# Kernel tuning notes

Measured on AMD Instinct MI355X. Metric: run time of the kernel, lower is better.

Reference implementation:

```python
import jax, jax.numpy as jnp
import numpy as np

N_NODES = 100000
N_EDGES = 1600000
IN = 128
HID = 128
OUT_CLS = 40
EPS = 1e-12


def setup_inputs() -> dict:
    key = jax.random.key(0)
    ks = jax.random.split(key, 12)
    feat = jax.random.normal(ks[0], (N_NODES, IN), dtype=jnp.float32)
    edge_index = jax.random.randint(ks[1], (2, N_EDGES), 0, N_NODES, dtype=jnp.int64)

    def xavier(k, shape):
        fan_out, fan_in = shape
        lim = float(np.sqrt(6.0 / (fan_in + fan_out)))
        return jax.random.uniform(k, shape, jnp.float32, -lim, lim)

    return {
        "feat": feat,
        "edge_index": edge_index,
        "Wl1": xavier(ks[2], (HID, IN)),  "bl1": jnp.zeros((HID,), jnp.float32), "Wr1": xavier(ks[3], (HID, IN)),
        "Wl2": xavier(ks[4], (HID, HID)), "bl2": jnp.zeros((HID,), jnp.float32), "Wr2": xavier(ks[5], (HID, HID)),
        "Wl3": xavier(ks[6], (HID, HID)), "bl3": jnp.zeros((HID,), jnp.float32), "Wr3": xavier(ks[7], (HID, HID)),
        "Wfc": xavier(ks[8], (OUT_CLS, HID)), "bfc": jnp.zeros((OUT_CLS,), jnp.float32),
    }


def sage_conv(x, src, dst, Wl, bl, Wr):
    # mean-aggregate neighbor messages x[src] into dst nodes (PyG aggr='mean')
    agg = jax.ops.segment_sum(x[src], dst, num_segments=N_NODES)        # [N, d]
    cnt = jax.ops.segment_sum(jnp.ones((src.shape[0],), x.dtype), dst,
                              num_segments=N_NODES)                      # [N]
    agg = agg / jnp.maximum(cnt, 1.0)[:, None]
    out = agg @ Wl.T + bl + x @ Wr.T                                     # lin_l(agg) + lin_r(x)
    # F.normalize(p=2, dim=-1, eps=1e-12)
    norm = jnp.linalg.norm(out, axis=-1, keepdims=True)
    return out / jnp.maximum(norm, EPS)


def reference(feat, edge_index, Wl1, bl1, Wr1, Wl2, bl2, Wr2, Wl3, bl3, Wr3, Wfc, bfc):
    src, dst = edge_index[0], edge_index[1]
    h = jax.nn.relu(sage_conv(feat, src, dst, Wl1, bl1, Wr1))
    h = jax.nn.relu(sage_conv(h, src, dst, Wl2, bl2, Wr2))
    h = sage_conv(h, src, dst, Wl3, bl3, Wr3)
    logits = h @ Wfc.T + bfc
    return jax.nn.softmax(logits, axis=-1)
```

## Files before the change

kernel.cpp:

```cpp
#include <hip/hip_runtime.h>
#include <cstdint>

#define N_NODES 100000
#define N_EDGES 1600000
#define F 128
#define OUT_CLS 40
#define LW 13
#define LBM (LW * 32)
#define BSHIFT 10
#define NBUCK 98
#define TILE 2048

using f32x16 = __attribute__((ext_vector_type(16))) float;
using bf16x8 = __attribute__((ext_vector_type(8))) short;
using f16x2 = __attribute__((ext_vector_type(2))) _Float16;

__device__ __forceinline__ int edge_val(const int* eb, int is64, long idx) {
  return is64 ? eb[2 * idx] : eb[idx];
}

__global__ void k_detect(const unsigned int* eb, int* flag) {
  if (threadIdx.x == 0 && blockIdx.x == 0) {
    int is64 = 1;
#pragma unroll
    for (int i = 1; i < 16; i += 2) is64 &= (eb[i] == 0u);
    flag[0] = is64;
  }
}

#define CH_E 16
__global__ __launch_bounds__(256) void k_chist(const int* __restrict__ eb, const int* __restrict__ flag,
                                               int* __restrict__ bhist) {
  __shared__ int lh[NBUCK];
  int t = threadIdx.x;
  if (t < NBUCK) lh[t] = 0;
  __syncthreads();
  int is64 = flag[0];
  long base = (long)blockIdx.x * (256 * CH_E);
#pragma unroll
  for (int i = 0; i < CH_E; ++i) {
    long e = base + (long)i * 256 + t;
    if (e < N_EDGES) {
      int d = edge_val(eb, is64, (long)N_EDGES + e);
      atomicAdd(&lh[d >> BSHIFT], 1);
    }
  }
  __syncthreads();
  if (t < NBUCK && lh[t]) atomicAdd(&bhist[t], lh[t]);
}

__global__ __launch_bounds__(128) void k_bscan(const int* __restrict__ bhist, int* __restrict__ boff,
                                               int* __restrict__ bkt_cursor, int* __restrict__ off) {
  __shared__ int sh[128];
  int t = threadIdx.x;
  int v = (t < NBUCK) ? bhist[t] : 0;
  sh[t] = v;
  __syncthreads();
  for (int d = 1; d < 128; d <<= 1) {
    int u = (t >= d) ? sh[t - d] : 0;
    __syncthreads();
    sh[t] += u;
    __syncthreads();
  }
  int incl = sh[t];
  if (t < NBUCK) {
    boff[t] = incl - v;
    bkt_cursor[t] = incl - v;
  }
  if (t == NBUCK - 1) boff[NBUCK] = incl;
  if (t == 0) off[N_NODES] = N_EDGES;
}

__global__ __launch_bounds__(256) void k_bscatter(const int* __restrict__ eb, const int* __restrict__ flag,
                                                  int* __restrict__ bkt_cursor, unsigned* __restrict__ ebuf) {
  __shared__ int lhist[128];
  __shared__ int lbase[128];
  __shared__ int gbase[NBUCK];
  __shared__ int lcnt[NBUCK];
  __shared__ unsigned buf[TILE];
  __shared__ int slotpos[TILE];
  int t = threadIdx.x;
  long e0 = (long)blockIdx.x * TILE;
  int is64 = flag[0];
  if (t < 128) lhist[t] = 0;
  __syncthreads();
#pragma unroll
  for (int i = 0; i < TILE / 256; ++i) {
    long e = e0 + t + i * 256;
    if (e < N_EDGES) {
      int d = edge_val(eb, is64, (long)N_EDGES + e);
      atomicAdd(&lhist[d >> BSHIFT], 1);
    }
  }
  __syncthreads();
  if (t < 128) lbase[t] = lhist[t];
  __syncthreads();
  for (int d = 1; d < 128; d <<= 1) {
    int v = (t >= d && t < 128) ? lbase[t - d] : 0;
    __syncthreads();
    if (t < 128) lbase[t] += v;
    __syncthreads();
  }
  if (t < NBUCK) {
    gbase[t] = atomicAdd(&bkt_cursor[t], lhist[t]);
    lcnt[t] = 0;
  }
  __syncthreads();
#pragma unroll
  for (int i = 0; i < TILE / 256; ++i) {
    long e = e0 + t + i * 256;
    if (e < N_EDGES) {
      int d = edge_val(eb, is64, (long)N_EDGES + e);
      int s = edge_val(eb, is64, e);
      int b = d >> BSHIFT;
      int n = atomicAdd(&lcnt[b], 1);
      int slot = lbase[b] - lhist[b] + n;
      buf[slot] = (unsigned)s | ((unsigned)(d & 1023) << 17);
      slotpos[slot] = gbase[b] + n;
    }
  }
  __syncthreads();
  int tile_n = (int)min((long)TILE, (long)N_EDGES - e0);
  for (int i = t; i < tile_n; i += 256) {
    ebuf[slotpos[i]] = buf[i];
  }
}

__global__ __launch_bounds__(1024) void k_fsort(const unsigned* __restrict__ ebuf, const int* __restrict__ boff,
                                                int* __restrict__ off, int* __restrict__ srcs) {
  __shared__ int hist[1024];
  __shared__ int cur[1024];
  __shared__ int wsum[16];
  int b = blockIdx.x;
  int t = threadIdx.x;
  int p0 = boff[b], p1 = boff[b + 1];
  hist[t] = 0;
  __syncthreads();
  for (int p = p0 + t; p < p1; p += 1024) {
    int d = (int)(ebuf[p] >> 17);
    atomicAdd(&hist[d], 1);
  }
  __syncthreads();
  int h = hist[t];
  int v = h;
#pragma unroll
  for (int o = 1; o < 64; o <<= 1) {
    int u = __shfl_up(v, o);
    if ((t & 63) >= o) v += u;
  }
  if ((t & 63) == 63) wsum[t >> 6] = v;
  __syncthreads();
  if (t < 64) {
    int w = (t < 16) ? wsum[t] : 0;
#pragma unroll
    for (int o = 1; o < 16; o <<= 1) {
      int u = __shfl_up(w, o);
      if (t >= o) w += u;
    }
    if (t < 16) wsum[t] = w;
  }
  __syncthreads();
  int base = (t >> 6) ? wsum[(t >> 6) - 1] : 0;
  int gpos = p0 + base + v - h;
  int node = (b << BSHIFT) + t;
  if (node < N_NODES) off[node] = gpos;
  cur[t] = gpos;
  __syncthreads();
  for (int p = p0 + t; p < p1; p += 1024) {
    unsigned e = ebuf[p];
    int pos = atomicAdd(&cur[(int)(e >> 17)], 1);
    srcs[pos] = (int)(e & 0x1FFFFu);
  }
}

__global__ __launch_bounds__(256) void k_tohalf(const float* __restrict__ in, _Float16* __restrict__ o) {
  int i = blockIdx.x * 256 + threadIdx.x;
  if (i >= N_NODES * F / 8) return;
  float4 a = reinterpret_cast<const float4*>(in)[2 * i];
  float4 b = reinterpret_cast<const float4*>(in)[2 * i + 1];
  union {
    _Float16 h[8];
    uint4 u;
  } r;
  r.h[0] = (_Float16)a.x; r.h[1] = (_Float16)a.y; r.h[2] = (_Float16)a.z; r.h[3] = (_Float16)a.w;
  r.h[4] = (_Float16)b.x; r.h[5] = (_Float16)b.y; r.h[6] = (_Float16)b.z; r.h[7] = (_Float16)b.w;
  reinterpret_cast<uint4*>(o)[i] = r.u;
}

__global__ __launch_bounds__(256) void k_aggregate(const _Float16* __restrict__ x, const int* __restrict__ off,
                                                   const int* __restrict__ srcs, float* __restrict__ agg) {
  int n = blockIdx.x * 4 + (threadIdx.x >> 6);
  if (n >= N_NODES) return;
  int l = threadIdx.x & 63;
  int p0 = off[n], p1 = off[n + 1];
  int deg = p1 - p0;
  float sx = 0.f, sy = 0.f;

  for (int base = 0; base < deg; base += 64) {
    int rem = deg - base;
    int cnt = (rem < 64) ? rem : 64;
    int my = (l < cnt) ? srcs[p0 + base + l] : 0;
    int j = 0;
    for (; j + 7 < cnt; j += 8) {
      int s[8];
#pragma unroll
      for (int k = 0; k < 8; ++k) s[k] = __builtin_amdgcn_readlane(my, j + k);
      f16x2 v[8];
#pragma unroll
      for (int k = 0; k < 8; ++k)
        v[k] = *reinterpret_cast<const f16x2*>(x + (size_t)(unsigned)s[k] * F + 2 * l);
#pragma unroll
      for (int k = 0; k < 8; ++k) {
        sx += (float)v[k][0];
        sy += (float)v[k][1];
      }
    }
    for (; j + 3 < cnt; j += 4) {
      int s[4];
#pragma unroll
      for (int k = 0; k < 4; ++k) s[k] = __builtin_amdgcn_readlane(my, j + k);
      f16x2 v[4];
#pragma unroll
      for (int k = 0; k < 4; ++k)
        v[k] = *reinterpret_cast<const f16x2*>(x + (size_t)(unsigned)s[k] * F + 2 * l);
#pragma unroll
      for (int k = 0; k < 4; ++k) {
        sx += (float)v[k][0];
        sy += (float)v[k][1];
      }
    }
    for (; j < cnt; ++j) {
      int s = __builtin_amdgcn_readlane(my, j);
      f16x2 v = *reinterpret_cast<const f16x2*>(x + (size_t)(unsigned)s * F + 2 * l);
      sx += (float)v[0];
      sy += (float)v[1];
    }
  }

  float inv = 1.0f / (float)max(deg, 1);
  float2 r;
  r.x = sx * inv;
  r.y = sy * inv;
  *reinterpret_cast<float2*>(agg + (size_t)n * F + 2 * l) = r;
}

__device__ __forceinline__ void split_pack(const float4& a, const float4& b, bf16x8& hi, bf16x8& lo) {
  float f[8] = {a.x, a.y, a.z, a.w, b.x, b.y, b.z, b.w};
#pragma unroll
  for (int i = 0; i < 8; ++i) {
    union { float f; unsigned u; } u0;
    u0.f = f[i];
    hi[i] = (short)(u0.u >> 16);
    union { unsigned u; float f; } uh;
    uh.u = u0.u & 0xFFFF0000u;
    union { float f; unsigned u; } ur;
    ur.f = f[i] - uh.f;
    lo[i] = (short)(ur.u >> 16);
  }
}

__global__ __launch_bounds__(256) void k_wsplit(const float* __restrict__ Wl1, const float* __restrict__ Wr1,
                                                const float* __restrict__ Wl2, const float* __restrict__ Wr2,
                                                const float* __restrict__ Wl3, const float* __restrict__ Wr3,
                                                unsigned short* __restrict__ wsp) {
  int e = blockIdx.x * 256 + threadIdx.x;
  if (e >= 3 * 16384) return;
  int L = e >> 14, off = e & 16383;
  const float* wl = (L == 0) ? Wl1 : (L == 1) ? Wl2 : Wl3;
  const float* wr = (L == 0) ? Wr1 : (L == 1) ? Wr2 : Wr3;
  unsigned short* base = wsp + (size_t)L * 4 * 16384;
  {
    union { float f; unsigned u; } u0;
    u0.f = wl[off];
    union { unsigned u; float f; } uh;
    uh.u = u0.u & 0xFFFF0000u;
    union { float f; unsigned u; } ur;
    ur.f = u0.f - uh.f;
    base[off] = (unsigned short)(u0.u >> 16);
    base[16384 + off] = (unsigned short)(ur.u >> 16);
  }
  {
    union { float f; unsigned u; } u0;
    u0.f = wr[off];
    union { unsigned u; float f; } uh;
    uh.u = u0.u & 0xFFFF0000u;
    union { float f; unsigned u; } ur;
    ur.f = u0.f - uh.f;
    base[2 * 16384 + off] = (unsigned short)(u0.u >> 16);
    base[3 * 16384 + off] = (unsigned short)(ur.u >> 16);
  }
}

__global__ __launch_bounds__(832, 1) void k_linear(const float* __restrict__ agg, const float* __restrict__ x,
                                                   const unsigned short* __restrict__ wsp,
                                                   const float* __restrict__ bl, float* out,
                                                   _Float16* __restrict__ out16, int relu) {
  __shared__ unsigned short wlds[4][128][136];
  int tid = threadIdx.x;

  for (int c = tid; c < 4 * 2048; c += 832) {
    int m = c >> 11, rem = c & 2047;
    int j = rem >> 4, kc = (rem & 15) * 8;
    uint4 v = *reinterpret_cast<const uint4*>(wsp + (size_t)m * 16384 + j * 128 + kc);
    *reinterpret_cast<uint4*>(&wlds[m][j][kc]) = v;
  }
  __syncthreads();

  int wid = tid >> 6, lane = tid & 63;
  int l31 = lane & 31, lhi = lane >> 5;
  long rb = (long)blockIdx.x * LBM + (long)wid * 32;
  if (rb >= N_NODES) return;

  int r0 = (int)min(rb + l31, (long)N_NODES - 1);
  const float* a0p = agg + (size_t)r0 * F + lhi * 8;
  const float* x0p = x + (size_t)r0 * F + lhi * 8;

  f32x16 acc[4];
#pragma unroll
  for (int ct = 0; ct < 4; ++ct) acc[ct] = (f32x16)0.f;

  float4 ap = *reinterpret_cast<const float4*>(a0p);
  float4 aq = *reinterpret_cast<const float4*>(a0p + 4);
  float4 xp = *reinterpret_cast<const float4*>(x0p);
  float4 xq = *reinterpret_cast<const float4*>(x0p + 4);

#pragma unroll
  for (int ks = 0; ks < 8; ++ks) {
    float4 ap_n, aq_n, xp_n, xq_n;
    if (ks < 7) {
      const float* an = a0p + (ks + 1) * 16;
      const float* xn = x0p + (ks + 1) * 16;
      ap_n = *reinterpret_cast<const float4*>(an);
      aq_n = *reinterpret_cast<const float4*>(an + 4);
      xp_n = *reinterpret_cast<const float4*>(xn);
      xq_n = *reinterpret_cast<const float4*>(xn + 4);
    }
    int k0 = ks * 16 + lhi * 8;
    bf16x8 aH0, aL0, xH0, xL0;
    split_pack(ap, aq, aH0, aL0);
    split_pack(xp, xq, xH0, xL0);
#pragma unroll
    for (int ct = 0; ct < 4; ++ct) {
      int j = ct * 32 + l31;
      bf16x8 BlH = *reinterpret_cast<const bf16x8*>(&wlds[0][j][k0]);
      bf16x8 BlL = *reinterpret_cast<const bf16x8*>(&wlds[1][j][k0]);
      bf16x8 BrH = *reinterpret_cast<const bf16x8*>(&wlds[2][j][k0]);
      bf16x8 BrL = *reinterpret_cast<const bf16x8*>(&wlds[3][j][k0]);
      acc[ct] = __builtin_amdgcn_mfma_f32_32x32x16_bf16(aH0, BlH, acc[ct], 0, 0, 0);
      acc[ct] = __builtin_amdgcn_mfma_f32_32x32x16_bf16(aL0, BlH, acc[ct], 0, 0, 0);
      acc[ct] = __builtin_amdgcn_mfma_f32_32x32x16_bf16(aH0, BlL, acc[ct], 0, 0, 0);
      acc[ct] = __builtin_amdgcn_mfma_f32_32x32x16_bf16(xH0, BrH, acc[ct], 0, 0, 0);
      acc[ct] = __builtin_amdgcn_mfma_f32_32x32x16_bf16(xL0, BrH, acc[ct], 0, 0, 0);
      acc[ct] = __builtin_amdgcn_mfma_f32_32x32x16_bf16(xH0, BrL, acc[ct], 0, 0, 0);
    }
    ap = ap_n;
    aq = aq_n;
    xp = xp_n;
    xq = xq_n;
  }

#pragma unroll
  for (int ct = 0; ct < 4; ++ct) {
    float b = bl[ct * 32 + l31];
#pragma unroll
    for (int i = 0; i < 16; ++i) acc[ct][i] += b;
  }
#pragma unroll
  for (int i = 0; i < 16; ++i) {
    float ss = acc[0][i] * acc[0][i] + acc[1][i] * acc[1][i] +
               acc[2][i] * acc[2][i] + acc[3][i] * acc[3][i];
#pragma unroll
    for (int o = 1; o < 32; o <<= 1) ss += __shfl_xor(ss, o);
    float inv = 1.0f / fmaxf(sqrtf(ss), 1e-12f);
    long grow = rb + (i & 3) + 8 * (i >> 2) + 4 * lhi;
    if (grow < N_NODES) {
      long base = grow * F + l31;
#pragma unroll
      for (int ct = 0; ct < 4; ++ct) {
        float v = acc[ct][i] * inv;
        if (relu) v = fmaxf(v, 0.f);
        out[base + ct * 32] = v;
        if (out16) out16[base + ct * 32] = (_Float16)v;
      }
    }
  }
}

#define FCP 132
__global__ __launch_bounds__(256) void k_fc_softmax(const float* __restrict__ h, const float* __restrict__ Wfc,
                                                    const float* __restrict__ bfc, float* __restrict__ out) {
  __shared__ float w_s[OUT_CLS][FCP];
  __shared__ float h_s[32][FCP];
  int tid = threadIdx.x;
  int nb = blockIdx.x * 32;

  for (int i = tid; i < OUT_CLS * (F / 4); i += 256) {
    int r = i >> 5, c = (i & 31) * 4;
    *reinterpret_cast<float4*>(&w_s[r][c]) = *reinterpret_cast<const float4*>(Wfc + (size_t)r * F + c);
  }
  for (int i = tid; i < 32 * (F / 4); i += 256) {
    int r = i >> 5, c = (i & 31) * 4;
    *reinterpret_cast<float4*>(&h_s[r][c]) = *reinterpret_cast<const float4*>(h + (size_t)(nb + r) * F + c);
  }
  __syncthreads();

  int r = tid >> 3, sub = tid & 7;
  float acc[5];
#pragma unroll
  for (int c = 0; c < 5; ++c) acc[c] = bfc[sub * 5 + c];

  for (int k4 = 0; k4 < F / 4; ++k4) {
    float4 hv = *reinterpret_cast<const float4*>(&h_s[r][k4 * 4]);
#pragma unroll
    for (int c = 0; c < 5; ++c) {
      float4 wv = *reinterpret_cast<const float4*>(&w_s[sub * 5 + c][k4 * 4]);
      acc[c] += hv.x * wv.x + hv.y * wv.y + hv.z * wv.z + hv.w * wv.w;
    }
  }

  float m = acc[0];
#pragma unroll
  for (int c = 1; c < 5; ++c) m = fmaxf(m, acc[c]);
#pragma unroll
  for (int o = 4; o > 0; o >>= 1) m = fmaxf(m, __shfl_xor(m, o));
  float e[5], s = 0.f;
#pragma unroll
  for (int c = 0; c < 5; ++c) {
    e[c] = expf(acc[c] - m);
    s += e[c];
  }
#pragma unroll
  for (int o = 4; o > 0; o >>= 1) s += __shfl_xor(s, o);
  float inv = 1.0f / s;
#pragma unroll
  for (int c = 0; c < 5; ++c) out[(size_t)(nb + r) * OUT_CLS + sub * 5 + c] = e[c] * inv;
}

extern "C" void kernel_launch(void* const* d_in, const int* in_sizes, int n_in, void* d_out, int out_size,
                              void* d_ws, size_t ws_size, hipStream_t stream) {
  const float* feat = (const float*)d_in[0];
  const int* eb = (const int*)d_in[1];
  const float* Wl1 = (const float*)d_in[2];
  const float* bl1 = (const float*)d_in[3];
  const float* Wr1 = (const float*)d_in[4];
  const float* Wl2 = (const float*)d_in[5];
  const float* bl2 = (const float*)d_in[6];
  const float* Wr2 = (const float*)d_in[7];
  const float* Wl3 = (const float*)d_in[8];
  const float* bl3 = (const float*)d_in[9];
  const float* Wr3 = (const float*)d_in[10];
  const float* Wfc = (const float*)d_in[11];
  const float* bfc = (const float*)d_in[12];
  float* out = (float*)d_out;

  char* w = (char*)d_ws;
  auto alloc = [&](size_t bytes) {
    char* p = w;
    w += (bytes + 255) & ~(size_t)255;
    return p;
  };
  int* flag = (int*)alloc(4);
  int* bhist = (int*)alloc((size_t)NBUCK * 4);
  int* boff = (int*)alloc((size_t)(NBUCK + 1) * 4);
  int* off = (int*)alloc((size_t)(N_NODES + 1) * 4);
  int* srcs = (int*)alloc((size_t)N_EDGES * 4 + 256);
  int* bkt_cursor = (int*)alloc((size_t)NBUCK * 4);
  unsigned short* wsp = (unsigned short*)alloc((size_t)3 * 4 * 16384 * 2);
  float* bufA = (float*)alloc((size_t)N_NODES * F * 4);
  float* bufB = (float*)alloc((size_t)N_NODES * F * 4);
  _Float16* h16X = (_Float16*)alloc((size_t)N_NODES * F * 2);
  _Float16* h16A = (_Float16*)alloc((size_t)N_NODES * F * 2);
  unsigned* ebuf = (unsigned*)bufB;
  (void)ws_size;
  (void)in_sizes;
  (void)n_in;
  (void)out_size;

  hipMemsetAsync(bhist, 0, (size_t)NBUCK * 4, stream);
  k_detect<<<1, 64, 0, stream>>>((const unsigned int*)eb, flag);
  k_chist<<<(N_EDGES + 256 * CH_E - 1) / (256 * CH_E), 256, 0, stream>>>(eb, flag, bhist);
  k_bscan<<<1, 128, 0, stream>>>(bhist, boff, bkt_cursor, off);
  k_bscatter<<<(N_EDGES + TILE - 1) / TILE, 256, 0, stream>>>(eb, flag, bkt_cursor, ebuf);
  k_fsort<<<NBUCK, 1024, 0, stream>>>(ebuf, boff, off, srcs);
  k_wsplit<<<192, 256, 0, stream>>>(Wl1, Wr1, Wl2, Wr2, Wl3, Wr3, wsp);
  k_tohalf<<<(N_NODES * F / 8 + 255) / 256, 256, 0, stream>>>(feat, h16X);

  const int nag = (N_NODES + 3) / 4;
  const int nlin = (N_NODES + LBM - 1) / LBM;
  const int nfc = N_NODES / 32;

  k_aggregate<<<nag, 256, 0, stream>>>(h16X, off, srcs, bufA);
  k_linear<<<nlin, 832, 0, stream>>>(bufA, feat, wsp + 0 * 4 * 16384, bl1, bufA, h16A, 1);
  k_aggregate<<<nag, 256, 0, stream>>>(h16A, off, srcs, bufB);
  k_linear<<<nlin, 832, 0, stream>>>(bufB, bufA, wsp + 1 * 4 * 16384, bl2, bufB, h16X, 1);
  k_aggregate<<<nag, 256, 0, stream>>>(h16X, off, srcs, bufA);
  k_linear<<<nlin, 832, 0, stream>>>(bufA, bufB, wsp + 2 * 4 * 16384, bl3, bufA, ((_Float16*)0), 0);
  k_fc_softmax<<<nfc, 256, 0, stream>>>(bufA, Wfc, bfc, out);
}
```

Before: 407.4 us.

## Fuse neighbor aggregation with SAGE linear layer via shared-memory staging

Merges the separate aggregate and linear kernels into one kernel per layer. Each block gathers and averages neighbor features for 128 nodes into shared memory, then runs the bf16-split MFMA linear layer reading the aggregate from LDS. This removes the fp32 aggregate round-trip through global memory and half the launches. In exchange, weights are now read from global/L2 instead of LDS, and aggregation parallelism drops, since each wave processes 32 nodes serially and occupancy is limited by the 67KB shared tile.

```diff
diff --git a/kernel.cpp b/kernel.cpp
--- a/kernel.cpp
+++ b/kernel.cpp
@@ -5,8 +5,7 @@
 #define N_EDGES 1600000
 #define F 128
 #define OUT_CLS 40
-#define LW 13
-#define LBM (LW * 32)
+#define FM 128
 #define BSHIFT 10
 #define NBUCK 98
 #define TILE 2048
@@ -185,63 +184,6 @@
   r.h[0] = (_Float16)a.x; r.h[1] = (_Float16)a.y; r.h[2] = (_Float16)a.z; r.h[3] = (_Float16)a.w;
   r.h[4] = (_Float16)b.x; r.h[5] = (_Float16)b.y; r.h[6] = (_Float16)b.z; r.h[7] = (_Float16)b.w;
   reinterpret_cast<uint4*>(o)[i] = r.u;
-}
-
-__global__ __launch_bounds__(256) void k_aggregate(const _Float16* __restrict__ x, const int* __restrict__ off,
-                                                   const int* __restrict__ srcs, float* __restrict__ agg) {
-  int n = blockIdx.x * 4 + (threadIdx.x >> 6);
-  if (n >= N_NODES) return;
-  int l = threadIdx.x & 63;
-  int p0 = off[n], p1 = off[n + 1];
-  int deg = p1 - p0;
-  float sx = 0.f, sy = 0.f;
-
-  for (int base = 0; base < deg; base += 64) {
-    int rem = deg - base;
-    int cnt = (rem < 64) ? rem : 64;
-    int my = (l < cnt) ? srcs[p0 + base + l] : 0;
-    int j = 0;
-    for (; j + 7 < cnt; j += 8) {
-      int s[8];
-#pragma unroll
-      for (int k = 0; k < 8; ++k) s[k] = __builtin_amdgcn_readlane(my, j + k);
-      f16x2 v[8];
-#pragma unroll
-      for (int k = 0; k < 8; ++k)
-        v[k] = *reinterpret_cast<const f16x2*>(x + (size_t)(unsigned)s[k] * F + 2 * l);
-#pragma unroll
-      for (int k = 0; k < 8; ++k) {
-        sx += (float)v[k][0];
-        sy += (float)v[k][1];
-      }
-    }
-    for (; j + 3 < cnt; j += 4) {
-      int s[4];
-#pragma unroll
-      for (int k = 0; k < 4; ++k) s[k] = __builtin_amdgcn_readlane(my, j + k);
-      f16x2 v[4];
-#pragma unroll
-      for (int k = 0; k < 4; ++k)
-        v[k] = *reinterpret_cast<const f16x2*>(x + (size_t)(unsigned)s[k] * F + 2 * l);
-#pragma unroll
-      for (int k = 0; k < 4; ++k) {
-        sx += (float)v[k][0];
-        sy += (float)v[k][1];
-      }
-    }
-    for (; j < cnt; ++j) {
-      int s = __builtin_amdgcn_readlane(my, j);
-      f16x2 v = *reinterpret_cast<const f16x2*>(x + (size_t)(unsigned)s * F + 2 * l);
-      sx += (float)v[0];
-      sy += (float)v[1];
-    }
-  }
-
-  float inv = 1.0f / (float)max(deg, 1);
-  float2 r;
-  r.x = sx * inv;
-  r.y = sy * inv;
-  *reinterpret_cast<float2*>(agg + (size_t)n * F + 2 * l) = r;
 }
 
 __device__ __forceinline__ void split_pack(const float4& a, const float4& b, bf16x8& hi, bf16x8& lo) {
@@ -291,61 +233,105 @@
   }
 }
 
-__global__ __launch_bounds__(832, 1) void k_linear(const float* __restrict__ agg, const float* __restrict__ x,
-                                                   const unsigned short* __restrict__ wsp,
-                                                   const float* __restrict__ bl, float* out,
-                                                   _Float16* __restrict__ out16, int relu) {
-  __shared__ unsigned short wlds[4][128][136];
+__global__ __launch_bounds__(256, 2) void k_fused(const _Float16* __restrict__ x16, const float* __restrict__ x,
+                                                  const int* __restrict__ off, const int* __restrict__ srcs,
+                                                  const unsigned short* __restrict__ wsp,
+                                                  const float* __restrict__ bl, float* __restrict__ out,
+                                                  _Float16* __restrict__ out16, int relu) {
+  __shared__ float agg_s[FM][132];
   int tid = threadIdx.x;
-
-  for (int c = tid; c < 4 * 2048; c += 832) {
-    int m = c >> 11, rem = c & 2047;
-    int j = rem >> 4, kc = (rem & 15) * 8;
-    uint4 v = *reinterpret_cast<const uint4*>(wsp + (size_t)m * 16384 + j * 128 + kc);
-    *reinterpret_cast<uint4*>(&wlds[m][j][kc]) = v;
-  }
-  __syncthreads();
-
   int wid = tid >> 6, lane = tid & 63;
+  long rb = (long)blockIdx.x * FM;
+
+  for (int i = 0; i < 32; ++i) {
+    long n = rb + wid * 32 + i;
+    if (n >= N_NODES) break;
+    int p0 = off[n], p1 = off[n + 1];
+    int deg = p1 - p0;
+    float sx = 0.f, sy = 0.f;
+    for (int base = 0; base < deg; base += 64) {
+      int rem = deg - base;
+      int cnt = (rem < 64) ? rem : 64;
+      int my = (lane < cnt) ? srcs[p0 + base + lane] : 0;
+      int j = 0;
+      for (; j + 7 < cnt; j += 8) {
+        int s[8];
+#pragma unroll
+        for (int k = 0; k < 8; ++k) s[k] = __builtin_amdgcn_readlane(my, j + k);
+        f16x2 v[8];
+#pragma unroll
+        for (int k = 0; k < 8; ++k)
+          v[k] = *reinterpret_cast<const f16x2*>(x16 + (size_t)(unsigned)s[k] * F + 2 * lane);
+#pragma unroll
+        for (int k = 0; k < 8; ++k) {
+          sx += (float)v[k][0];
+          sy += (float)v[k][1];
+        }
+      }
+      for (; j + 3 < cnt; j += 4) {
+        int s[4];
+#pragma unroll
+        for (int k = 0; k < 4; ++k) s[k] = __builtin_amdgcn_readlane(my, j + k);
+        f16x2 v[4];
+#pragma unroll
+        for (int k = 0; k < 4; ++k)
+          v[k] = *reinterpret_cast<const f16x2*>(x16 + (size_t)(unsigned)s[k] * F + 2 * lane);
+#pragma unroll
+        for (int k = 0; k < 4; ++k) {
+          sx += (float)v[k][0];
+          sy += (float)v[k][1];
+        }
+      }
+      for (; j < cnt; ++j) {
+        int s = __builtin_amdgcn_readlane(my, j);
+        f16x2 v = *reinterpret_cast<const f16x2*>(x16 + (size_t)(unsigned)s * F + 2 * lane);
+        sx += (float)v[0];
+        sy += (float)v[1];
+      }
+    }
+    float inv = 1.0f / (float)max(deg, 1);
+    float2 r;
+    r.x = sx * inv;
+    r.y = sy * inv;
+    *reinterpret_cast<float2*>(&agg_s[wid * 32 + i][2 * lane]) = r;
+  }
+  __syncthreads();
+
   int l31 = lane & 31, lhi = lane >> 5;
-  long rb = (long)blockIdx.x * LBM + (long)wid * 32;
-  if (rb >= N_NODES) return;
-
-  int r0 = (int)min(rb + l31, (long)N_NODES - 1);
-  const float* a0p = agg + (size_t)r0 * F + lhi * 8;
+  int lrow = wid * 32 + l31;
+  long rbw = rb + wid * 32;
+  int r0 = (int)min(rbw + l31, (long)N_NODES - 1);
   const float* x0p = x + (size_t)r0 * F + lhi * 8;
 
   f32x16 acc[4];
 #pragma unroll
   for (int ct = 0; ct < 4; ++ct) acc[ct] = (f32x16)0.f;
 
-  float4 ap = *reinterpret_cast<const float4*>(a0p);
-  float4 aq = *reinterpret_cast<const float4*>(a0p + 4);
   float4 xp = *reinterpret_cast<const float4*>(x0p);
   float4 xq = *reinterpret_cast<const float4*>(x0p + 4);
 
 #pragma unroll
   for (int ks = 0; ks < 8; ++ks) {
-    float4 ap_n, aq_n, xp_n, xq_n;
+    float4 xp_n, xq_n;
     if (ks < 7) {
-      const float* an = a0p + (ks + 1) * 16;
       const float* xn = x0p + (ks + 1) * 16;
-      ap_n = *reinterpret_cast<const float4*>(an);
-      aq_n = *reinterpret_cast<const float4*>(an + 4);
       xp_n = *reinterpret_cast<const float4*>(xn);
       xq_n = *reinterpret_cast<const float4*>(xn + 4);
     }
     int k0 = ks * 16 + lhi * 8;
+    float4 ap = *reinterpret_cast<const float4*>(&agg_s[lrow][k0]);
+    float4 aq = *reinterpret_cast<const float4*>(&agg_s[lrow][k0 + 4]);
     bf16x8 aH0, aL0, xH0, xL0;
     split_pack(ap, aq, aH0, aL0);
     split_pack(xp, xq, xH0, xL0);
 #pragma unroll
     for (int ct = 0; ct < 4; ++ct) {
       int j = ct * 32 + l31;
-      bf16x8 BlH = *reinterpret_cast<const bf16x8*>(&wlds[0][j][k0]);
-      bf16x8 BlL = *reinterpret_cast<const bf16x8*>(&wlds[1][j][k0]);
-      bf16x8 BrH = *reinterpret_cast<const bf16x8*>(&wlds[2][j][k0]);
-      bf16x8 BrL = *reinterpret_cast<const bf16x8*>(&wlds[3][j][k0]);
+      const unsigned short* wb = wsp + (size_t)j * 128 + k0;
+      bf16x8 BlH = *reinterpret_cast<const bf16x8*>(wb);
+      bf16x8 BlL = *reinterpret_cast<const bf16x8*>(wb + 16384);
+      bf16x8 BrH = *reinterpret_cast<const bf16x8*>(wb + 2 * 16384);
+      bf16x8 BrL = *reinterpret_cast<const bf16x8*>(wb + 3 * 16384);
       acc[ct] = __builtin_amdgcn_mfma_f32_32x32x16_bf16(aH0, BlH, acc[ct], 0, 0, 0);
       acc[ct] = __builtin_amdgcn_mfma_f32_32x32x16_bf16(aL0, BlH, acc[ct], 0, 0, 0);
       acc[ct] = __builtin_amdgcn_mfma_f32_32x32x16_bf16(aH0, BlL, acc[ct], 0, 0, 0);
@@ -353,8 +339,6 @@
       acc[ct] = __builtin_amdgcn_mfma_f32_32x32x16_bf16(xL0, BrH, acc[ct], 0, 0, 0);
       acc[ct] = __builtin_amdgcn_mfma_f32_32x32x16_bf16(xH0, BrL, acc[ct], 0, 0, 0);
     }
-    ap = ap_n;
-    aq = aq_n;
     xp = xp_n;
     xq = xq_n;
   }
@@ -372,7 +356,7 @@
 #pragma unroll
     for (int o = 1; o < 32; o <<= 1) ss += __shfl_xor(ss, o);
     float inv = 1.0f / fmaxf(sqrtf(ss), 1e-12f);
-    long grow = rb + (i & 3) + 8 * (i >> 2) + 4 * lhi;
+    long grow = rbw + (i & 3) + 8 * (i >> 2) + 4 * lhi;
     if (grow < N_NODES) {
       long base = grow * F + l31;
 #pragma unroll
@@ -485,15 +469,11 @@
   k_wsplit<<<192, 256, 0, stream>>>(Wl1, Wr1, Wl2, Wr2, Wl3, Wr3, wsp);
   k_tohalf<<<(N_NODES * F / 8 + 255) / 256, 256, 0, stream>>>(feat, h16X);
 
-  const int nag = (N_NODES + 3) / 4;
-  const int nlin = (N_NODES + LBM - 1) / LBM;
+  const int nfu = (N_NODES + FM - 1) / FM;
   const int nfc = N_NODES / 32;
 
-  k_aggregate<<<nag, 256, 0, stream>>>(h16X, off, srcs, bufA);
-  k_linear<<<nlin, 832, 0, stream>>>(bufA, feat, wsp + 0 * 4 * 16384, bl1, bufA, h16A, 1);
-  k_aggregate<<<nag, 256, 0, stream>>>(h16A, off, srcs, bufB);
-  k_linear<<<nlin, 832, 0, stream>>>(bufB, bufA, wsp + 1 * 4 * 16384, bl2, bufB, h16X, 1);
-  k_aggregate<<<nag, 256, 0, stream>>>(h16X, off, srcs, bufA);
-  k_linear<<<nlin, 832, 0, stream>>>(bufA, bufB, wsp + 2 * 4 * 16384, bl3, bufA, ((_Float16*)0), 0);
+  k_fused<<<nfu, 256, 0, stream>>>(h16X, feat, off, srcs, wsp + 0 * 4 * 16384, bl1, bufA, h16A, 1);
+  k_fused<<<nfu, 256, 0, stream>>>(h16A, bufA, off, srcs, wsp + 1 * 4 * 16384, bl2, bufB, h16X, 1);
+  k_fused<<<nfu, 256, 0, stream>>>(h16X, bufB, off, srcs, wsp + 2 * 4 * 16384, bl3, bufA, ((_Float16*)0), 0);
   k_fc_softmax<<<nfc, 256, 0, stream>>>(bufA, Wfc, bfc, out);
 }
```

Result: slower. 766.4 us (+88.1%).
